# Kernel tuning notes

Hardware: AMD Instinct MI355X
Metric: run time of the kernel (lower is better)

## Reference

```python
import jax, jax.numpy as jnp
import numpy as np

KSIZE = 3
RES_SCALE = 0.2
WITH_RESIDUAL = True


def setup_inputs() -> dict:
    key = jax.random.key(0)
    x = jax.random.normal(key, (8, 3, 1024, 1024), dtype=jnp.float32)
    return {"x": x}


def reference(x) -> jnp.ndarray:
    B, C, H, W = x.shape
    k = KSIZE
    p = k // 2
    # zero padding matches F.unfold(padding=k//2)
    xp = jnp.pad(x, ((0, 0), (0, 0), (p, p), (p, p)))
    # [B, C, k*k, H, W] stack of shifted views (k*k = 9, small static loop)
    patches = jnp.stack(
        [xp[:, :, di:di + H, dj:dj + W] for di in range(k) for dj in range(k)],
        axis=2,
    )
    # median of odd-sized window = middle element of sorted values
    med = jnp.sort(patches, axis=2)[:, :, (k * k) // 2]
    if WITH_RESIDUAL:
        return x + RES_SCALE * (med - x)
    return med
```

## Files before the change

kernel.cpp:

```cpp
#include <hip/hip_runtime.h>


typedef float v4f __attribute__((ext_vector_type(4)));

#define S2(a,b) { float _t=fminf(a,b); (b)=fmaxf(a,b); (a)=_t; }
__device__ __forceinline__ float med3f(float a,float b,float c){
    return fmaxf(fminf(a,b), fminf(fmaxf(a,b),c));
}

constexpr int W = 1024, H = 1024;
constexpr int R = 8;
constexpr int NL = R + 2;

__global__ __launch_bounds__(256, 2) void median_blur_kernel(
    const float* __restrict__ xin, float* __restrict__ out)
{
    __shared__ float eL[NL][4];
    __shared__ float eR[NL][4];

    const int tx   = threadIdx.x;
    const int lane = tx & 63;
    const int wv   = tx >> 6;
    const int x0   = tx << 2;
    const int y0   = blockIdx.x * R;
    const size_t plane = (size_t)blockIdx.y * H * W;
    const float* base  = xin + plane;
    float*       obase = out + plane;

    v4f row[NL];
#pragma unroll
    for (int s = 0; s < NL; ++s) {
        int y = y0 - 1 + s;
        y = y < 0 ? 0 : (y > H - 1 ? H - 1 : y);
        row[s] = *reinterpret_cast<const v4f*>(base + (size_t)y * W + x0);
    }
    {
        float* rf = reinterpret_cast<float*>(row);
#pragma unroll
        for (int i = 0; i < NL * 4; ++i) asm volatile("" : "+v"(rf[i]));
    }

    if (lane == 0) {
#pragma unroll
        for (int s = 0; s < NL; ++s) eL[s][wv] = row[s].x;
    }
    if (lane == 63) {
#pragma unroll
        for (int s = 0; s < NL; ++s) eR[s][wv] = row[s].w;
    }
    __syncthreads();

    float rr[NL][6];
#pragma unroll
    for (int s = 0; s < NL; ++s) {
        const int y = y0 - 1 + s;
        const bool valid = (y >= 0) && (y < H);
        v4f c = row[s];
        float l = __shfl_up(c.w, 1);
        float r = __shfl_down(c.x, 1);
        if (lane == 0)  l = (wv > 0) ? eR[s][wv - 1] : 0.0f;
        if (lane == 63) r = (wv < 3) ? eL[s][wv + 1] : 0.0f;
        rr[s][0] = valid ? l   : 0.0f;
        rr[s][1] = valid ? c.x : 0.0f;
        rr[s][2] = valid ? c.y : 0.0f;
        rr[s][3] = valid ? c.z : 0.0f;
        rr[s][4] = valid ? c.w : 0.0f;
        rr[s][5] = valid ? r   : 0.0f;
    }

#pragma unroll
    for (int r = 0; r < R; ++r) {
        const float* t  = rr[r];
        const float* mm = rr[r + 1];
        const float* bb = rr[r + 2];
        float lo[6], mi[6], hi[6];
#pragma unroll
        for (int j = 0; j < 6; ++j) {
            float a = t[j], c0 = mm[j], d = bb[j];
            S2(a, c0); S2(c0, d); S2(a, c0);
            lo[j] = a; mi[j] = c0; hi[j] = d;
        }
        v4f o;
#pragma unroll
        for (int j = 0; j < 4; ++j) {
            float mxlo = fmaxf(lo[j], fmaxf(lo[j + 1], lo[j + 2]));
            float mnhi = fminf(hi[j], fminf(hi[j + 1], hi[j + 2]));
            float mdmi = med3f(mi[j], mi[j + 1], mi[j + 2]);
            float med  = med3f(mxlo, mdmi, mnhi);
            float xc   = mm[j + 1];
            o[j] = xc + 0.2f * (med - xc);
        }
        __builtin_nontemporal_store(o,
            reinterpret_cast<v4f*>(obase + (size_t)(y0 + r) * W + x0));
    }
}

extern "C" void kernel_launch(void* const* d_in, const int* in_sizes, int n_in,
                              void* d_out, int out_size, void* d_ws, size_t ws_size,
                              hipStream_t stream) {
    const float* x = (const float*)d_in[0];
    float* out = (float*)d_out;
    const int planes = in_sizes[0] / (H * W);
    dim3 block(256);
    dim3 grid(H / R, planes);
    median_blur_kernel<<<grid, block, 0, stream>>>(x, out);
}
```

Before: 175.9 us.

## Stream rows through a rolling register ring and load halo columns directly

Each block now handles 16 rows instead of 8. The block keeps a 6-slot rotating ring of rows in registers and prefetches rows several iterations ahead of the compute, instead of loading all rows up front. The left and right halo pixels are read straight from global memory (cache hits), which replaces the LDS edge exchange, the lane shuffles and the __syncthreads. Launch bounds are raised to 6 waves per SIMD to increase occupancy. In exchange there are extra scalar loads per row and more loop iterations per block.

```diff
diff --git a/kernel.cpp b/kernel.cpp
--- a/kernel.cpp
+++ b/kernel.cpp
@@ -4,94 +4,99 @@
 typedef float v4f __attribute__((ext_vector_type(4)));
 
 #define S2(a,b) { float _t=fminf(a,b); (b)=fmaxf(a,b); (a)=_t; }
-__device__ __forceinline__ float med3f(float a,float b,float c){
-    return fmaxf(fminf(a,b), fminf(fmaxf(a,b),c));
+
+__device__ __forceinline__ float med3f(float a, float b, float c) {
+    return fmaxf(fminf(a, b), fminf(fmaxf(a, b), c));
+}
+__device__ __forceinline__ float max3f(float a, float b, float c) {
+    return fmaxf(a, fmaxf(b, c));
+}
+__device__ __forceinline__ float min3f(float a, float b, float c) {
+    return fminf(a, fminf(b, c));
 }
 
-constexpr int W = 1024, H = 1024;
-constexpr int R = 8;
-constexpr int NL = R + 2;
+constexpr int W  = 1024, H = 1024;
+constexpr int RS = 16;
+constexpr int P  = 6;
 
-__global__ __launch_bounds__(256, 2) void median_blur_kernel(
+__global__ __launch_bounds__(256, 6) void median_blur_kernel(
     const float* __restrict__ xin, float* __restrict__ out)
 {
-    __shared__ float eL[NL][4];
-    __shared__ float eR[NL][4];
-
-    const int tx   = threadIdx.x;
-    const int lane = tx & 63;
-    const int wv   = tx >> 6;
-    const int x0   = tx << 2;
-    const int y0   = blockIdx.x * R;
-    const size_t plane = (size_t)blockIdx.y * H * W;
+    const int tx = threadIdx.x;
+    const int x0 = tx << 2;
+    const int y0 = (int)blockIdx.x * RS;
+    const size_t plane = (size_t)blockIdx.y * (size_t)(H * W);
     const float* base  = xin + plane;
     float*       obase = out + plane;
 
-    v4f row[NL];
+    const bool lE = (tx == 0);
+    const bool rE = (tx == 255);
+    const int  xl = lE ? x0       : x0 - 1;
+    const int  xr = rE ? x0 + 3   : x0 + 4;
+
+    v4f   cc[P];
+    float ll[P], rr[P];
+
+    const v4f vz = {0.0f, 0.0f, 0.0f, 0.0f};
+
 #pragma unroll
-    for (int s = 0; s < NL; ++s) {
-        int y = y0 - 1 + s;
-        y = y < 0 ? 0 : (y > H - 1 ? H - 1 : y);
-        row[s] = *reinterpret_cast<const v4f*>(base + (size_t)y * W + x0);
-    }
-    {
-        float* rf = reinterpret_cast<float*>(row);
-#pragma unroll
-        for (int i = 0; i < NL * 4; ++i) asm volatile("" : "+v"(rf[i]));
-    }
-
-    if (lane == 0) {
-#pragma unroll
-        for (int s = 0; s < NL; ++s) eL[s][wv] = row[s].x;
-    }
-    if (lane == 63) {
-#pragma unroll
-        for (int s = 0; s < NL; ++s) eR[s][wv] = row[s].w;
-    }
-    __syncthreads();
-
-    float rr[NL][6];
-#pragma unroll
-    for (int s = 0; s < NL; ++s) {
+    for (int s = 0; s < P - 1; ++s) {
         const int y = y0 - 1 + s;
-        const bool valid = (y >= 0) && (y < H);
-        v4f c = row[s];
-        float l = __shfl_up(c.w, 1);
-        float r = __shfl_down(c.x, 1);
-        if (lane == 0)  l = (wv > 0) ? eR[s][wv - 1] : 0.0f;
-        if (lane == 63) r = (wv < 3) ? eL[s][wv + 1] : 0.0f;
-        rr[s][0] = valid ? l   : 0.0f;
-        rr[s][1] = valid ? c.x : 0.0f;
-        rr[s][2] = valid ? c.y : 0.0f;
-        rr[s][3] = valid ? c.z : 0.0f;
-        rr[s][4] = valid ? c.w : 0.0f;
-        rr[s][5] = valid ? r   : 0.0f;
+        if (s == 0 && y < 0) {
+            cc[s] = vz; ll[s] = 0.0f; rr[s] = 0.0f;
+        } else {
+            const float* rp = base + ((size_t)y << 10);
+            cc[s] = *reinterpret_cast<const v4f*>(rp + x0);
+            ll[s] = rp[xl];
+            rr[s] = rp[xr];
+        }
     }
 
 #pragma unroll
-    for (int r = 0; r < R; ++r) {
-        const float* t  = rr[r];
-        const float* mm = rr[r + 1];
-        const float* bb = rr[r + 2];
+    for (int i = 0; i < RS; ++i) {
+        if (i + P - 1 <= RS + 1) {
+            const int s    = i + P - 1;
+            const int slot = s % P;
+            const int y    = y0 - 1 + s;
+            if (s == RS + 1 && y >= H) {
+                cc[slot] = vz; ll[slot] = 0.0f; rr[slot] = 0.0f;
+            } else {
+                const float* rp = base + ((size_t)y << 10);
+                cc[slot] = *reinterpret_cast<const v4f*>(rp + x0);
+                ll[slot] = rp[xl];
+                rr[slot] = rp[xr];
+            }
+            __builtin_amdgcn_sched_barrier(0);
+        }
+
+        const int sT = i % P, sM = (i + 1) % P, sB = (i + 2) % P;
+
+        const float t0 = lE ? 0.0f : ll[sT], t5 = rE ? 0.0f : rr[sT];
+        const float m0 = lE ? 0.0f : ll[sM], m5 = rE ? 0.0f : rr[sM];
+        const float b0 = lE ? 0.0f : ll[sB], b5 = rE ? 0.0f : rr[sB];
+        const float t[6] = { t0, cc[sT].x, cc[sT].y, cc[sT].z, cc[sT].w, t5 };
+        const float m[6] = { m0, cc[sM].x, cc[sM].y, cc[sM].z, cc[sM].w, m5 };
+        const float b[6] = { b0, cc[sB].x, cc[sB].y, cc[sB].z, cc[sB].w, b5 };
+
         float lo[6], mi[6], hi[6];
 #pragma unroll
         for (int j = 0; j < 6; ++j) {
-            float a = t[j], c0 = mm[j], d = bb[j];
+            float a = t[j], c0 = m[j], d = b[j];
             S2(a, c0); S2(c0, d); S2(a, c0);
             lo[j] = a; mi[j] = c0; hi[j] = d;
         }
         v4f o;
 #pragma unroll
         for (int j = 0; j < 4; ++j) {
-            float mxlo = fmaxf(lo[j], fmaxf(lo[j + 1], lo[j + 2]));
-            float mnhi = fminf(hi[j], fminf(hi[j + 1], hi[j + 2]));
-            float mdmi = med3f(mi[j], mi[j + 1], mi[j + 2]);
-            float med  = med3f(mxlo, mdmi, mnhi);
-            float xc   = mm[j + 1];
+            const float mxlo = max3f(lo[j], lo[j + 1], lo[j + 2]);
+            const float mnhi = min3f(hi[j], hi[j + 1], hi[j + 2]);
+            const float mdmi = med3f(mi[j], mi[j + 1], mi[j + 2]);
+            const float med  = med3f(mxlo, mdmi, mnhi);
+            const float xc   = m[j + 1];
             o[j] = xc + 0.2f * (med - xc);
         }
         __builtin_nontemporal_store(o,
-            reinterpret_cast<v4f*>(obase + (size_t)(y0 + r) * W + x0));
+            reinterpret_cast<v4f*>(obase + ((size_t)(y0 + i) << 10) + x0));
     }
 }
 
@@ -102,6 +107,6 @@
     float* out = (float*)d_out;
     const int planes = in_sizes[0] / (H * W);
     dim3 block(256);
-    dim3 grid(H / R, planes);
+    dim3 grid(H / RS, planes);
     median_blur_kernel<<<grid, block, 0, stream>>>(x, out);
 }
```

Measured after the change: 174.9 us. No clear change (-0.6%).
